# Kernel optimization log

Hardware: AMD Instinct MI355X
Metric: run time of the kernel (lower is better)

Reference implementation:

```python
import jax, jax.numpy as jnp
import numpy as np

SCALE = 16.0 / 8  # alpha / rank

def setup_inputs() -> dict:
    key = jax.random.key(0)
    k1, k2, k3, k4 = jax.random.split(key, 4)
    B, S, D_IN, D_OUT, R = 4, 2048, 4096, 4096, 8
    x = jax.random.normal(k1, (B, S, D_IN), dtype=jnp.float32)
    weight = jax.random.normal(k2, (D_OUT, D_IN), dtype=jnp.float32) * (1.0 / np.sqrt(D_IN))
    lora_A = jax.random.normal(k3, (R, D_IN), dtype=jnp.float32) * (1.0 / np.sqrt(D_IN))
    lora_B = jax.random.normal(k4, (D_OUT, R), dtype=jnp.float32) * 0.01
    return {"x": x, "weight": weight, "lora_A": lora_A, "lora_B": lora_B}

def reference(x, weight, lora_A, lora_B):
    # base: x @ W^T  -> [B, S, out]
    base_out = jnp.einsum('bsd,od->bso', x, weight)
    # low-rank path, chained as (x @ A^T) @ B^T (same math as x @ (B@A)^T)
    xa = jnp.einsum('bsd,rd->bsr', x, lora_A)      # [B, S, r]
    lora_out = jnp.einsum('bsr,or->bso', xa, lora_B)  # [B, S, out]
    return base_out + SCALE * lora_out
```

## Files before the change

kernel.cpp:

```cpp
#include <hip/hip_runtime.h>
#include <hip/hip_bf16.h>

typedef unsigned short u16;
typedef __attribute__((ext_vector_type(8))) __bf16 bf16x8;
typedef __attribute__((ext_vector_type(4))) float f32x4;
typedef __attribute__((ext_vector_type(8))) unsigned short ushort8;

#define GM 8192
#define GN 4096
#define GK 4096
#define NT (GK / 64)

__device__ __forceinline__ u16 f2bf(float f) {
  unsigned u = __float_as_uint(f);
  u += 0x7fffu + ((u >> 16) & 1u);
  return (u16)(u >> 16);
}

__global__ void build_weff(const float* __restrict__ W,
                           const float* __restrict__ lA,
                           const float* __restrict__ lB,
                           u16* __restrict__ Weff) {
  const int o = blockIdx.x;
  float b[8];
#pragma unroll
  for (int r = 0; r < 8; ++r) b[r] = 2.0f * lB[o * 8 + r];
  const float* wrow = W + (size_t)o * GK;
  u16* orow = Weff + (size_t)o * GK;
  for (int d = threadIdx.x * 4; d < GK; d += blockDim.x * 4) {
    float4 w = *reinterpret_cast<const float4*>(wrow + d);
    float a0 = w.x, a1 = w.y, a2 = w.z, a3 = w.w;
#pragma unroll
    for (int r = 0; r < 8; ++r) {
      float4 a = *reinterpret_cast<const float4*>(lA + r * GK + d);
      a0 += b[r] * a.x; a1 += b[r] * a.y; a2 += b[r] * a.z; a3 += b[r] * a.w;
    }
    ushort4 p;
    p.x = f2bf(a0); p.y = f2bf(a1); p.z = f2bf(a2); p.w = f2bf(a3);
    *reinterpret_cast<ushort4*>(orow + d) = p;
  }
}

__global__ void cvt_bf16(const float* __restrict__ x, u16* __restrict__ xb) {
  const size_t i = ((size_t)blockIdx.x * blockDim.x + threadIdx.x) * 8;
  float4 v0 = *reinterpret_cast<const float4*>(x + i);
  float4 v1 = *reinterpret_cast<const float4*>(x + i + 4);
  ushort8 o;
  o[0] = f2bf(v0.x); o[1] = f2bf(v0.y); o[2] = f2bf(v0.z); o[3] = f2bf(v0.w);
  o[4] = f2bf(v1.x); o[5] = f2bf(v1.y); o[6] = f2bf(v1.z); o[7] = f2bf(v1.w);
  *reinterpret_cast<ushort8*>(xb + i) = o;
}

__device__ __forceinline__ void gload16(const u16* g, u16* l) {
  __builtin_amdgcn_global_load_lds(
      (const __attribute__((address_space(1))) void*)g,
      (__attribute__((address_space(3))) void*)l, 16, 0, 0);
}

#define BAR()                                  \
  do {                                         \
    asm volatile("" ::: "memory");             \
    __builtin_amdgcn_s_barrier();              \
    asm volatile("" ::: "memory");             \
  } while (0)

__global__ __launch_bounds__(512, 2) void gemm256(const u16* __restrict__ Ab,
                                                  const u16* __restrict__ Bb,
                                                  float* __restrict__ C) {
  __shared__ u16 lds[2][2][256 * 64];

  const int tid = threadIdx.x;
  const int wv = tid >> 6;
  const int l = tid & 63;

  const int nwg = gridDim.x;
  const int cpx = nwg >> 3;
  const int wg = ((int)blockIdx.x & 7) * cpx + ((int)blockIdx.x >> 3);
  const int tm = wg >> 4;
  const int tn = wg & 15;

  const int wr = wv >> 2;
  const int wc = wv & 3;

  const int srow = (wv << 3) + (l >> 3);
  const int srl = ((wv & 1) << 3) | (l >> 3);
  const int skel = ((l & 7) << 3) ^ ((srl & 0xE) << 2);
  const u16* aG = Ab + (size_t)(tm * 256) * GK;
  const u16* bG = Bb + (size_t)(tn * 256) * GK;

  const int frow = l & 15;
  const int fksw = ((l >> 4) << 3) ^ ((frow & 0xE) << 2);
  const int arow = wr * 128 + frow;
  const int brow = wc * 64 + frow;

  auto STAGE = [&](int th, int r) {
    const int k0 = th << 6;
    const u16* src = (r < 2 ? aG : bG) +
                     (size_t)((r & 1) * 128 + srow) * GK + k0 + skel;
    u16* dst = &lds[th & 1][r >> 1][(r & 1) * 8192 + wv * 512];
#pragma unroll
    for (int j = 0; j < 2; ++j)
      gload16(src + (size_t)(j * 64) * GK, dst + j * 4096);
  };

  STAGE(0, 0); STAGE(0, 1); STAGE(0, 2); STAGE(0, 3);

  f32x4 acc[8][4] = {};
  bf16x8 af_lo[4][2], af_hi[4][2], bfr0[2][2], bfr1[2][2];

  for (int t = 0; t < NT; ++t) {
    asm volatile("s_waitcnt vmcnt(0)" ::: "memory");
    BAR();

    const u16* A = &lds[t & 1][0][0];
    const u16* B = &lds[t & 1][1][0];

#pragma unroll
    for (int n = 0; n < 2; ++n)
#pragma unroll
      for (int s = 0; s < 2; ++s)
        bfr0[n][s] = *reinterpret_cast<const bf16x8*>(
            B + (brow + n * 16) * 64 + (fksw ^ (s << 5)));
#pragma unroll
    for (int m = 0; m < 4; ++m)
#pragma unroll
      for (int s = 0; s < 2; ++s)
        af_lo[m][s] = *reinterpret_cast<const bf16x8*>(
            A + (arow + m * 16) * 64 + (fksw ^ (s << 5)));
#pragma unroll
    for (int n = 0; n < 2; ++n)
#pragma unroll
      for (int s = 0; s < 2; ++s)
        bfr1[n][s] = *reinterpret_cast<const bf16x8*>(
            B + (brow + (n + 2) * 16) * 64 + (fksw ^ (s << 5)));
#pragma unroll
    for (int m = 0; m < 4; ++m)
#pragma unroll
      for (int s = 0; s < 2; ++s)
        af_hi[m][s] = *reinterpret_cast<const bf16x8*>(
            A + (arow + (m + 4) * 16) * 64 + (fksw ^ (s << 5)));

    if (t + 1 < NT) {
      STAGE(t + 1, 0); STAGE(t + 1, 1); STAGE(t + 1, 2); STAGE(t + 1, 3);
    }

    __builtin_amdgcn_s_setprio(1);
#pragma unroll
    for (int m = 0; m < 4; ++m)
#pragma unroll
      for (int n = 0; n < 2; ++n)
#pragma unroll
        for (int s = 0; s < 2; ++s)
          acc[m][n] = __builtin_amdgcn_mfma_f32_16x16x32_bf16(
              af_lo[m][s], bfr0[n][s], acc[m][n], 0, 0, 0);
#pragma unroll
    for (int m = 0; m < 4; ++m)
#pragma unroll
      for (int n = 0; n < 2; ++n)
#pragma unroll
        for (int s = 0; s < 2; ++s)
          acc[m][n + 2] = __builtin_amdgcn_mfma_f32_16x16x32_bf16(
              af_lo[m][s], bfr1[n][s], acc[m][n + 2], 0, 0, 0);
#pragma unroll
    for (int m = 0; m < 4; ++m)
#pragma unroll
      for (int n = 0; n < 2; ++n)
#pragma unroll
        for (int s = 0; s < 2; ++s)
          acc[m + 4][n + 2] = __builtin_amdgcn_mfma_f32_16x16x32_bf16(
              af_hi[m][s], bfr1[n][s], acc[m + 4][n + 2], 0, 0, 0);
#pragma unroll
    for (int m = 0; m < 4; ++m)
#pragma unroll
      for (int n = 0; n < 2; ++n)
#pragma unroll
        for (int s = 0; s < 2; ++s)
          acc[m + 4][n] = __builtin_amdgcn_mfma_f32_16x16x32_bf16(
              af_hi[m][s], bfr0[n][s], acc[m + 4][n], 0, 0, 0);
    __builtin_amdgcn_s_setprio(0);
  }

  const int orow = tm * 256 + wr * 128 + ((l >> 4) << 2);
  const int ocol = tn * 256 + wc * 64 + (l & 15);
#pragma unroll
  for (int m = 0; m < 8; ++m)
#pragma unroll
    for (int n = 0; n < 4; ++n) {
      float* cp = C + (size_t)(orow + m * 16) * GN + (ocol + n * 16);
#pragma unroll
      for (int j = 0; j < 4; ++j) cp[(size_t)j * GN] = acc[m][n][j];
    }
}

extern "C" void kernel_launch(void* const* d_in, const int* in_sizes, int n_in,
                              void* d_out, int out_size, void* d_ws, size_t ws_size,
                              hipStream_t stream) {
  const float* x  = (const float*)d_in[0];
  const float* W  = (const float*)d_in[1];
  const float* lA = (const float*)d_in[2];
  const float* lB = (const float*)d_in[3];
  float* out = (float*)d_out;

  u16* weff = (u16*)d_ws;
  u16* xb = (u16*)((char*)d_ws + (size_t)GN * GK * sizeof(u16));

  build_weff<<<GN, 256, 0, stream>>>(W, lA, lB, weff);
  cvt_bf16<<<(size_t)GM * GK / (256 * 8), 256, 0, stream>>>(x, xb);
  gemm256<<<(GM / 256) * (GN / 256), 512, 0, stream>>>(xb, weff, out);
}
```

Before: 292.2 us.

## Fuse fp32-to-bf16 conversion of x into GEMM A-tile staging

Removes the separate cvt_bf16 pass over x. The GEMM now reads fp32 x directly into registers, converts it to bf16 and writes it to swizzled LDS in the middle of the MFMA sequence. B tiles still use direct global-to-LDS loads, and the barrier moves to the end of each iteration. This avoids writing and rereading a 64 MB bf16 copy of x, but the GEMM now reads twice as many A bytes per tile (fp32), and each of the 16 column tiles rereads x, with extra register pressure and VALU conversion work inside the loop.

```diff
diff --git a/kernel.cpp b/kernel.cpp
--- a/kernel.cpp
+++ b/kernel.cpp
@@ -41,16 +41,6 @@
   }
 }
 
-__global__ void cvt_bf16(const float* __restrict__ x, u16* __restrict__ xb) {
-  const size_t i = ((size_t)blockIdx.x * blockDim.x + threadIdx.x) * 8;
-  float4 v0 = *reinterpret_cast<const float4*>(x + i);
-  float4 v1 = *reinterpret_cast<const float4*>(x + i + 4);
-  ushort8 o;
-  o[0] = f2bf(v0.x); o[1] = f2bf(v0.y); o[2] = f2bf(v0.z); o[3] = f2bf(v0.w);
-  o[4] = f2bf(v1.x); o[5] = f2bf(v1.y); o[6] = f2bf(v1.z); o[7] = f2bf(v1.w);
-  *reinterpret_cast<ushort8*>(xb + i) = o;
-}
-
 __device__ __forceinline__ void gload16(const u16* g, u16* l) {
   __builtin_amdgcn_global_load_lds(
       (const __attribute__((address_space(1))) void*)g,
@@ -64,7 +54,7 @@
     asm volatile("" ::: "memory");             \
   } while (0)
 
-__global__ __launch_bounds__(512, 2) void gemm256(const u16* __restrict__ Ab,
+__global__ __launch_bounds__(512, 2) void gemm256(const float* __restrict__ X,
                                                   const u16* __restrict__ Bb,
                                                   float* __restrict__ C) {
   __shared__ u16 lds[2][2][256 * 64];
@@ -85,7 +75,7 @@
   const int srow = (wv << 3) + (l >> 3);
   const int srl = ((wv & 1) << 3) | (l >> 3);
   const int skel = ((l & 7) << 3) ^ ((srl & 0xE) << 2);
-  const u16* aG = Ab + (size_t)(tm * 256) * GK;
+  const float* xG = X + (size_t)(tm * 256) * GK;
   const u16* bG = Bb + (size_t)(tn * 256) * GK;
 
   const int frow = l & 15;
@@ -93,25 +83,60 @@
   const int arow = wr * 128 + frow;
   const int brow = wc * 64 + frow;
 
-  auto STAGE = [&](int th, int r) {
-    const int k0 = th << 6;
-    const u16* src = (r < 2 ? aG : bG) +
-                     (size_t)((r & 1) * 128 + srow) * GK + k0 + skel;
-    u16* dst = &lds[th & 1][r >> 1][(r & 1) * 8192 + wv * 512];
+  auto STAGE_B = [&](int th, int r) {
+    const int tc = th < NT ? th : NT - 1;
+    const int k0 = tc << 6;
+    const u16* src = bG + (size_t)(r * 128 + srow) * GK + k0 + skel;
+    u16* dst = &lds[th & 1][1][r * 8192 + wv * 512];
 #pragma unroll
     for (int j = 0; j < 2; ++j)
       gload16(src + (size_t)(j * 64) * GK, dst + j * 4096);
   };
 
-  STAGE(0, 0); STAGE(0, 1); STAGE(0, 2); STAGE(0, 3);
+  const int acol = (l & 7) * 8;
+  auto STAGE_A_LOAD = [&](int th, float4* v) {
+    const int tc = th < NT ? th : NT - 1;
+    const int k0 = tc << 6;
+#pragma unroll
+    for (int p = 0; p < 4; ++p) {
+      const float* src = xG + (size_t)(p * 64 + srow) * GK + k0 + acol;
+      v[p * 2 + 0] = *reinterpret_cast<const float4*>(src);
+      v[p * 2 + 1] = *reinterpret_cast<const float4*>(src + 4);
+    }
+  };
+  auto STAGE_A_WRITE = [&](int th, const float4* v) {
+#pragma unroll
+    for (int p = 0; p < 4; ++p) {
+      const int row = p * 64 + srow;
+      u16* dst = &lds[th & 1][0][row * 64 + (acol ^ ((row & 0xE) << 2))];
+      const float4 v0 = v[p * 2 + 0], v1 = v[p * 2 + 1];
+      __hip_bfloat162 q0 = __float22bfloat162_rn(make_float2(v0.x, v0.y));
+      __hip_bfloat162 q1 = __float22bfloat162_rn(make_float2(v0.z, v0.w));
+      __hip_bfloat162 q2 = __float22bfloat162_rn(make_float2(v1.x, v1.y));
+      __hip_bfloat162 q3 = __float22bfloat162_rn(make_float2(v1.z, v1.w));
+      uint4 pk;
+      pk.x = *reinterpret_cast<const unsigned*>(&q0);
+      pk.y = *reinterpret_cast<const unsigned*>(&q1);
+      pk.z = *reinterpret_cast<const unsigned*>(&q2);
+      pk.w = *reinterpret_cast<const unsigned*>(&q3);
+      *reinterpret_cast<uint4*>(dst) = pk;
+    }
+  };
+
+  {
+    STAGE_B(0, 0); STAGE_B(0, 1);
+    float4 av[8];
+    STAGE_A_LOAD(0, av);
+    asm volatile("s_waitcnt vmcnt(0)" ::: "memory");
+    STAGE_A_WRITE(0, av);
+    asm volatile("s_waitcnt lgkmcnt(0)" ::: "memory");
+    BAR();
+  }
 
   f32x4 acc[8][4] = {};
   bf16x8 af_lo[4][2], af_hi[4][2], bfr0[2][2], bfr1[2][2];
 
   for (int t = 0; t < NT; ++t) {
-    asm volatile("s_waitcnt vmcnt(0)" ::: "memory");
-    BAR();
-
     const u16* A = &lds[t & 1][0][0];
     const u16* B = &lds[t & 1][1][0];
 
@@ -140,9 +165,9 @@
         af_hi[m][s] = *reinterpret_cast<const bf16x8*>(
             A + (arow + (m + 4) * 16) * 64 + (fksw ^ (s << 5)));
 
-    if (t + 1 < NT) {
-      STAGE(t + 1, 0); STAGE(t + 1, 1); STAGE(t + 1, 2); STAGE(t + 1, 3);
-    }
+    STAGE_B(t + 1, 0); STAGE_B(t + 1, 1);
+    float4 av[8];
+    STAGE_A_LOAD(t + 1, av);
 
     __builtin_amdgcn_s_setprio(1);
 #pragma unroll
@@ -161,6 +186,12 @@
         for (int s = 0; s < 2; ++s)
           acc[m][n + 2] = __builtin_amdgcn_mfma_f32_16x16x32_bf16(
               af_lo[m][s], bfr1[n][s], acc[m][n + 2], 0, 0, 0);
+    __builtin_amdgcn_s_setprio(0);
+
+    asm volatile("s_waitcnt vmcnt(0)" ::: "memory");
+    STAGE_A_WRITE(t + 1, av);
+
+    __builtin_amdgcn_s_setprio(1);
 #pragma unroll
     for (int m = 0; m < 4; ++m)
 #pragma unroll
@@ -178,6 +209,9 @@
           acc[m + 4][n] = __builtin_amdgcn_mfma_f32_16x16x32_bf16(
               af_hi[m][s], bfr0[n][s], acc[m + 4][n], 0, 0, 0);
     __builtin_amdgcn_s_setprio(0);
+
+    asm volatile("s_waitcnt lgkmcnt(0)" ::: "memory");
+    BAR();
   }
 
   const int orow = tm * 256 + wr * 128 + ((l >> 4) << 2);
@@ -202,9 +236,7 @@
   float* out = (float*)d_out;
 
   u16* weff = (u16*)d_ws;
-  u16* xb = (u16*)((char*)d_ws + (size_t)GN * GK * sizeof(u16));
 
   build_weff<<<GN, 256, 0, stream>>>(W, lA, lB, weff);
-  cvt_bf16<<<(size_t)GM * GK / (256 * 8), 256, 0, stream>>>(x, xb);
-  gemm256<<<(GM / 256) * (GN / 256), 512, 0, stream>>>(xb, weff, out);
-}
+  gemm256<<<(GM / 256) * (GN / 256), 512, 0, stream>>>(x, weff, out);
+}
```

Result: slower. 640.0 us (+119.0%).
